# Kernel tuning notes

Hardware: AMD Instinct MI355X
Metric: run time of the kernel (lower is better)

The kernel has to match this reference:

```python
import jax, jax.numpy as jnp
import numpy as np

B, S, D = 1, 2048, 2048
H, G, HD = 32, 8, 64
EPS = 1e-6
ROPE_BASE = 10000.0


def rms_norm(x, g):
    # torch RMSNorm computed in fp32 then cast back (PytorchRMSNorm wrapper)
    xf = x.astype(jnp.float32)
    y = xf * jax.lax.rsqrt(jnp.mean(xf * xf, axis=-1, keepdims=True) + EPS) * g.astype(jnp.float32)
    return y.astype(x.dtype)


def rotate_half(x):
    x1, x2 = jnp.split(x, 2, axis=-1)
    return jnp.concatenate([-x2, x1], axis=-1)


def apply_rope(x, cos, sin):
    # x: (b, h, s, hd); cos/sin: (s, hd)
    return x * cos[None, None] + rotate_half(x) * sin[None, None]


def setup_inputs() -> dict:
    key = jax.random.key(0)
    ks = jax.random.split(key, 8)
    x = jax.random.normal(ks[0], (B, S, D), dtype=jnp.float32)
    wq = jax.random.normal(ks[1], (H * HD, D), dtype=jnp.float32) * (D ** -0.5)
    wk = jax.random.normal(ks[2], (G * HD, D), dtype=jnp.float32) * (D ** -0.5)
    wv = jax.random.normal(ks[3], (G * HD, D), dtype=jnp.float32) * (D ** -0.5)
    wo = jax.random.normal(ks[4], (D, H * HD), dtype=jnp.float32) * (D ** -0.5)
    qg = jnp.ones((HD,), dtype=jnp.float32)
    kg = jnp.ones((HD,), dtype=jnp.float32)
    # RoPE tables (HF-style: duplicated half-dim frequencies)
    inv_freq = 1.0 / (ROPE_BASE ** (jnp.arange(0, HD, 2, dtype=jnp.float32) / HD))
    ang = jnp.arange(S, dtype=jnp.float32)[:, None] * inv_freq[None, :]  # (S, HD/2)
    emb = jnp.concatenate([ang, ang], axis=-1)  # (S, HD)
    cos = jnp.cos(emb)
    sin = jnp.sin(emb)
    # causal mask: True = future (upper-right triangle)
    mask = jnp.triu(jnp.ones((S, S), dtype=bool), k=1)
    return {"x": x, "mask": mask, "cos": cos, "sin": sin,
            "wq": wq, "wk": wk, "wv": wv, "wo": wo, "qg": qg, "kg": kg}


def reference(x, mask, cos, sin, wq, wk, wv, wo, qg, kg):
    b, s, _ = x.shape
    rep = H // G
    q = (x @ wq.T).reshape(b, s, H, HD).transpose(0, 2, 1, 3)   # (b,H,s,hd)
    k = (x @ wk.T).reshape(b, s, G, HD).transpose(0, 2, 1, 3)   # (b,G,s,hd)
    v = (x @ wv.T).reshape(b, s, G, HD).transpose(0, 2, 1, 3)
    q = rms_norm(q, qg)
    k = rms_norm(k, kg)
    q = apply_rope(q, cos[:s], sin[:s])
    k = apply_rope(k, cos[:s], sin[:s])
    k = jnp.repeat(k, rep, axis=1)  # (b,H,s,hd) GQA expansion
    v = jnp.repeat(v, rep, axis=1)
    scores = jnp.einsum('bhqd,bhkd->bhqk', q, k) * (HD ** -0.5)
    neg = jnp.finfo(scores.dtype).min / 2
    scores = jnp.where(mask[None, None, :s, :s], neg, scores)
    w = jax.nn.softmax(scores, axis=-1)
    ctx = jnp.einsum('bhqk,bhkd->bhqd', w, v)
    ctx = ctx.transpose(0, 2, 1, 3).reshape(b, s, H * HD)
    return ctx @ wo.T
```

## Files before the change

kernel.cpp:

```cpp
#include <hip/hip_runtime.h>
#include <stdint.h>

#define SEQ    2048
#define DMODEL 2048
#define NHEAD  32
#define NKV    8
#define HDIM   64
#define NQKV   3072

typedef __bf16 bf16x8 __attribute__((ext_vector_type(8)));
typedef float  f32x4  __attribute__((ext_vector_type(4)));

#define SCALE2 0.180336880f
#define THR2   12.0f

__device__ __forceinline__ ushort bf(float f){
  __bf16 h = (__bf16)f;
  return __builtin_bit_cast(unsigned short, h);
}

__device__ __forceinline__ void gl_lds16(const void* g, void* l){
  __builtin_amdgcn_global_load_lds(
      (const __attribute__((address_space(1))) uint32_t*)g,
      (__attribute__((address_space(3))) uint32_t*)l, 16, 0, 0);
}

__global__ __launch_bounds__(256) void k_cvt_all(const float* __restrict__ x,
                                                 const float* __restrict__ wq,
                                                 const float* __restrict__ wk,
                                                 const float* __restrict__ wv,
                                                 const float* __restrict__ wo,
                                                 ushort* __restrict__ xb,
                                                 ushort* __restrict__ wcat,
                                                 ushort* __restrict__ wob){
  int i = blockIdx.x * 256 + threadIdx.x;
  const float* src; ushort* dst; int s4; int d4;
  if (i < 1048576)      { src = x;  dst = xb;   s4 = i;           d4 = s4; }
  else if (i < 2097152) { src = wq; dst = wcat; s4 = i - 1048576; d4 = s4; }
  else if (i < 2359296) { src = wk; dst = wcat; s4 = i - 2097152; d4 = s4 + 1048576; }
  else if (i < 2621440) { src = wv; dst = wcat; s4 = i - 2359296; d4 = s4 + 1310720; }
  else                  { src = wo; dst = wob;  s4 = i - 2621440; d4 = s4; }
  float4 v = reinterpret_cast<const float4*>(src)[s4];
  ushort4 o;
  o.x = bf(v.x); o.y = bf(v.y); o.z = bf(v.z); o.w = bf(v.w);
  reinterpret_cast<ushort4*>(dst)[d4] = o;
}

__global__ __launch_bounds__(256) void k_gemm_bt(const ushort* __restrict__ A,
                                                 const ushort* __restrict__ B,
                                                 float* __restrict__ C,
                                                 int M, int N, int K){
  __shared__ ushort As[2][128*64];
  __shared__ ushort Bs[2][128*64];
  const int tid = threadIdx.x, lane = tid & 63, wid = tid >> 6;
  const int bm = blockIdx.y * 128, bn = blockIdx.x * 128;
  const int wr = wid >> 1, wc = wid & 1;
  const int l15 = lane & 15, u = lane >> 4;

  const int srow = wid*32 + (lane >> 3);
  const int scol = ((lane & 7) ^ (lane >> 3)) * 8;
  const ushort* Abase = A + (size_t)(bm + srow) * K + scol;
  const ushort* Bbase = B + (size_t)(bn + srow) * K + scol;

  auto STAGE = [&](int buf, int k0){
#pragma unroll
    for (int c = 0; c < 4; c++){
      gl_lds16(Abase + k0 + (size_t)c*8*K, &As[buf][(wid*32 + c*8)*64]);
      gl_lds16(Bbase + k0 + (size_t)c*8*K, &Bs[buf][(wid*32 + c*8)*64]);
    }
  };

  f32x4 acc[4][4] = {};
  const int NT = K >> 6;

  STAGE(0, 0);
  __syncthreads();

  for (int t = 0; t < NT; t++){
    const int cur = t & 1;
    if (t + 1 < NT) STAGE(cur ^ 1, (t + 1) << 6);

#pragma unroll
    for (int kc = 0; kc < 2; kc++){
      bf16x8 af[4], bfr[4];
#pragma unroll
      for (int m = 0; m < 4; m++){
        int row = wr*64 + m*16 + l15;
        af[m] = *reinterpret_cast<const bf16x8*>(&As[cur][row*64 + (((kc*4+u) ^ (row&7))*8)]);
      }
#pragma unroll
      for (int n = 0; n < 4; n++){
        int row = wc*64 + n*16 + l15;
        bfr[n] = *reinterpret_cast<const bf16x8*>(&Bs[cur][row*64 + (((kc*4+u) ^ (row&7))*8)]);
      }
      __builtin_amdgcn_s_setprio(1);
#pragma unroll
      for (int m = 0; m < 4; m++)
#pragma unroll
        for (int n = 0; n < 4; n++)
          acc[m][n] = __builtin_amdgcn_mfma_f32_16x16x32_bf16(af[m], bfr[n], acc[m][n], 0, 0, 0);
      __builtin_amdgcn_s_setprio(0);
    }

    __syncthreads();
  }

#pragma unroll
  for (int m = 0; m < 4; m++)
#pragma unroll
    for (int n = 0; n < 4; n++)
#pragma unroll
      for (int j = 0; j < 4; j++){
        int row = bm + wr*64 + m*16 + u*4 + j;
        int col = bn + wc*64 + n*16 + l15;
        C[(size_t)row * N + col] = acc[m][n][j];
      }
}

__global__ __launch_bounds__(256) void k_normrope(const float* __restrict__ qkv,
                                                  const float* __restrict__ cosp,
                                                  const float* __restrict__ sinp,
                                                  const float* __restrict__ qg,
                                                  const float* __restrict__ kg,
                                                  ushort* __restrict__ qb,
                                                  ushort* __restrict__ kb){
  const int s = blockIdx.x;
  const int tid = threadIdx.x, lane = tid & 63, wid = tid >> 6;
  const float* row = qkv + (size_t)s * NQKV;
  const float cs = cosp[s*HDIM + lane];
  const float sn = sinp[s*HDIM + lane];

  for (int hidx = wid; hidx < 40; hidx += 4){
    const bool isq = hidx < 32;
    const int col = isq ? hidx*64 : 2048 + (hidx-32)*64;
    float x = row[col + lane];
    float ss = x * x;
#pragma unroll
    for (int m = 1; m < 64; m <<= 1) ss += __shfl_xor(ss, m);
    float r = rsqrtf(ss * (1.0f/64.0f) + 1e-6f);
    float y = x * r * (isq ? qg : kg)[lane];
    float p = __shfl_xor(y, 32);
    float out = y * cs + (lane < 32 ? -p : p) * sn;
    if (isq) qb[(size_t)s*2048 + hidx*64 + lane] = bf(out * SCALE2);
    else     kb[(size_t)s*512 + (hidx-32)*64 + lane] = bf(out);
  }
}

__global__ __launch_bounds__(256) void k_vtrans(const float* __restrict__ qkvf,
                                                ushort* __restrict__ vtb){
  __shared__ ushort tile[64][68];
  const int g = blockIdx.x >> 5, st = blockIdx.x & 31;
  const int tid = threadIdx.x;
#pragma unroll
  for (int i = 0; i < 4; i++){
    int idx = i*256 + tid;
    int r = idx >> 4, c4 = idx & 15;
    float4 v = *reinterpret_cast<const float4*>(
        qkvf + (size_t)(st*64 + r)*NQKV + 2560 + g*64 + c4*4);
    tile[c4*4+0][r] = bf(v.x);
    tile[c4*4+1][r] = bf(v.y);
    tile[c4*4+2][r] = bf(v.z);
    tile[c4*4+3][r] = bf(v.w);
  }
  __syncthreads();
#pragma unroll
  for (int i = 0; i < 4; i++){
    int idx = i*256 + tid;
    int d = idx >> 4, s4 = idx & 15;
    int pos4 = (s4 >> 3)*32 + (s4 & 3)*8 + ((s4 >> 2) & 1)*4;
    ushort4 o = *reinterpret_cast<const ushort4*>(&tile[d][s4*4]);
    *reinterpret_cast<ushort4*>(vtb + (size_t)(g*64 + d)*SEQ + st*64 + pos4) = o;
  }
}

__global__ __launch_bounds__(256) void k_attn(const ushort* __restrict__ qbuf,
                                              const ushort* __restrict__ kbuf,
                                              const ushort* __restrict__ vtb,
                                              ushort* __restrict__ ctx){
  __shared__ ushort Kd[2][64*64];
  __shared__ ushort Vd[2][64*64];

  const int bx = blockIdx.x;
  const int h  = bx & 31;
  const int qt = 31 - (bx >> 5);
  const int g = h >> 2;
  const int tid = threadIdx.x, lane = tid & 63, wid = tid >> 6;
  const int l15 = lane & 15, u = lane >> 4;
  const int q0 = qt*64 + wid*16;
  const int tmax = qt;

  bf16x8 qf[2];
#pragma unroll
  for (int kc = 0; kc < 2; kc++)
    qf[kc] = *reinterpret_cast<const bf16x8*>(
        qbuf + (size_t)(q0 + l15)*2048 + h*64 + kc*32 + u*8);

  f32x4 o[4] = {};
  float mrun = -1e30f;
  float lrun = 0.f;

  const int srow = wid*16 + (lane >> 3);
  const int scol = ((lane & 7) ^ (lane >> 3)) * 8;
  const ushort* ksrc0 = kbuf + (size_t)srow*512 + g*64 + scol;
  const ushort* vsrc0 = vtb  + (size_t)(g*64 + srow)*SEQ + scol;

  auto STAGE = [&](int buf, int t){
    const ushort* ks = ksrc0 + (size_t)t*64*512;
    gl_lds16(ks,         &Kd[buf][wid*1024]);
    gl_lds16(ks + 8*512, &Kd[buf][wid*1024 + 512]);
    const ushort* vs = vsrc0 + t*64;
    gl_lds16(vs,          &Vd[buf][wid*1024]);
    gl_lds16(vs + 8*SEQ,  &Vd[buf][wid*1024 + 512]);
  };

  STAGE(0, 0);
  __syncthreads();

  for (int t = 0; t <= tmax; t++){
    const int cur = t & 1;
    if (t < tmax) STAGE(cur ^ 1, t + 1);

    const ushort* Kb = &Kd[cur][0];
    const ushort* Vb = &Vd[cur][0];
    const bool full = (t*64 + 63) <= q0;

    f32x4 st[4];
#pragma unroll
    for (int kb = 0; kb < 4; kb++){
      const int key0 = t*64 + kb*16;
      const int keyl = kb*16 + l15;
      if (key0 <= q0 + 15){
        bf16x8 kf0 = *reinterpret_cast<const bf16x8*>(&Kb[keyl*64 + ((u     ^ (keyl&7))*8)]);
        bf16x8 kf1 = *reinterpret_cast<const bf16x8*>(&Kb[keyl*64 + (((4|u) ^ (keyl&7))*8)]);
        f32x4 a = {};
        a = __builtin_amdgcn_mfma_f32_16x16x32_bf16(kf0, qf[0], a, 0, 0, 0);
        a = __builtin_amdgcn_mfma_f32_16x16x32_bf16(kf1, qf[1], a, 0, 0, 0);
        st[kb] = a;
      } else {
        st[kb] = (f32x4){-1e30f, -1e30f, -1e30f, -1e30f};
      }
    }
    if (!full){
      const int keyb = t*64 + u*4;
      const int qr = q0 + l15;
#pragma unroll
      for (int kb = 0; kb < 4; kb++)
#pragma unroll
        for (int j = 0; j < 4; j++)
          st[kb][j] = (keyb + kb*16 + j > qr) ? -1e30f : st[kb][j];
    }

    {
      f32x4 mx = st[0];
#pragma unroll
      for (int kb = 1; kb < 4; kb++)
#pragma unroll
        for (int j = 0; j < 4; j++) mx[j] = fmaxf(mx[j], st[kb][j]);
      float tml = fmaxf(fmaxf(mx[0], mx[1]), fmaxf(mx[2], mx[3]));
      if (__any(tml > mrun + THR2)){
        float tm = fmaxf(tml, __shfl_xor(tml, 16));
        tm = fmaxf(tm, __shfl_xor(tm, 32));
        float mn = fmaxf(mrun, tm);
        float al = exp2f(mrun - mn);
        mrun = mn;
        lrun *= al;
#pragma unroll
        for (int d0 = 0; d0 < 4; d0++)
#pragma unroll
          for (int j = 0; j < 4; j++) o[d0][j] *= al;
      }

#pragma unroll
      for (int kb = 0; kb < 4; kb++)
#pragma unroll
        for (int j = 0; j < 4; j++){
          float p = exp2f(st[kb][j] - mrun);
          st[kb][j] = p;
          lrun += p;
        }
    }

    __builtin_amdgcn_s_setprio(1);
#pragma unroll
    for (int kc = 0; kc < 2; kc++){
      bf16x8 pb;
#pragma unroll
      for (int e = 0; e < 4; e++){
        pb[e]   = (__bf16)st[2*kc  ][e];
        pb[4+e] = (__bf16)st[2*kc+1][e];
      }
#pragma unroll
      for (int d0 = 0; d0 < 4; d0++){
        const int vrow = d0*16 + l15;
        bf16x8 vb8 = *reinterpret_cast<const bf16x8*>(
            &Vb[vrow*64 + (((kc*4+u) ^ (vrow&7))*8)]);
        o[d0] = __builtin_amdgcn_mfma_f32_16x16x32_bf16(vb8, pb, o[d0], 0, 0, 0);
      }
    }
    __builtin_amdgcn_s_setprio(0);

    __syncthreads();
  }

  {
    float lt = lrun + __shfl_xor(lrun, 16);
    lt += __shfl_xor(lt, 32);
    float inv = 1.0f / lt;
#pragma unroll
    for (int d0 = 0; d0 < 4; d0++){
      ushort4 w;
      w.x = bf(o[d0][0] * inv); w.y = bf(o[d0][1] * inv);
      w.z = bf(o[d0][2] * inv); w.w = bf(o[d0][3] * inv);
      *reinterpret_cast<ushort4*>(
          &ctx[(size_t)(q0 + l15)*2048 + h*64 + d0*16 + u*4]) = w;
    }
  }
}

extern "C" void kernel_launch(void* const* d_in, const int* in_sizes, int n_in,
                              void* d_out, int out_size, void* d_ws, size_t ws_size,
                              hipStream_t stream){
  const float* x    = (const float*)d_in[0];
  const float* cosp = (const float*)d_in[2];
  const float* sinp = (const float*)d_in[3];
  const float* wq   = (const float*)d_in[4];
  const float* wk   = (const float*)d_in[5];
  const float* wv   = (const float*)d_in[6];
  const float* wo   = (const float*)d_in[7];
  const float* qg   = (const float*)d_in[8];
  const float* kg   = (const float*)d_in[9];
  float* out = (float*)d_out;

  char* ws = (char*)d_ws;
  ushort* xb   = (ushort*)(ws);
  ushort* wcat = (ushort*)(ws + 8388608);
  ushort* wob  = (ushort*)(ws + 20971520);
  float*  qkvf = (float* )(ws + 29360128);
  ushort* qb   = (ushort*)(ws + 54525952);
  ushort* kb   = (ushort*)(ws + 62914560);
  ushort* vtb  = (ushort*)(ws + 65011712);
  ushort* ctxb = (ushort*)(ws + 67108864);

  k_cvt_all<<<14336, 256, 0, stream>>>(x, wq, wk, wv, wo, xb, wcat, wob);
  k_gemm_bt<<<dim3(24, 16), 256, 0, stream>>>(xb, wcat, qkvf, 2048, 3072, 2048);
  k_normrope<<<2048, 256, 0, stream>>>(qkvf, cosp, sinp, qg, kg, qb, kb);
  k_vtrans<<<256, 256, 0, stream>>>(qkvf, vtb);
  k_attn<<<1024, 256, 0, stream>>>(qb, kb, vtb, ctxb);
  k_gemm_bt<<<dim3(16, 16), 256, 0, stream>>>(ctxb, wob, out, 2048, 2048, 2048);
}
```

Measured before the change: 150.5 us.

## Store QKV projection in bf16, rebalance attention tile order, precompute LDS offsets

Adds a bf16-output variant of the QKV GEMM so the intermediate buffer is half the size, and updates normrope and vtrans to read bf16. This cuts global write and read traffic for the 2048x3072 intermediate, at the cost of rounding q/k to bf16 before RMSNorm. The attention kernel also gets a new block-to-query-tile mapping that interleaves long and short causal tiles for load balance. It also precomputes LDS fragment offsets and uses packed v_cvt_pk_bf16_f32 for the P conversion.

```diff
diff --git a/kernel.cpp b/kernel.cpp
--- a/kernel.cpp
+++ b/kernel.cpp
@@ -17,6 +17,9 @@
 __device__ __forceinline__ ushort bf(float f){
   __bf16 h = (__bf16)f;
   return __builtin_bit_cast(unsigned short, h);
+}
+__device__ __forceinline__ float b2f(ushort v){
+  union { uint32_t u; float f; } a; a.u = ((uint32_t)v) << 16; return a.f;
 }
 
 __device__ __forceinline__ void gl_lds16(const void* g, void* l){
@@ -117,7 +120,78 @@
       }
 }
 
-__global__ __launch_bounds__(256) void k_normrope(const float* __restrict__ qkv,
+__global__ __launch_bounds__(256) void k_gemm_btc(const ushort* __restrict__ A,
+                                                  const ushort* __restrict__ B,
+                                                  ushort* __restrict__ C,
+                                                  int M, int N, int K){
+  __shared__ ushort As[2][128*64];
+  __shared__ ushort Bs[2][128*64];
+  const int tid = threadIdx.x, lane = tid & 63, wid = tid >> 6;
+  const int bm = blockIdx.y * 128, bn = blockIdx.x * 128;
+  const int wr = wid >> 1, wc = wid & 1;
+  const int l15 = lane & 15, u = lane >> 4;
+
+  const int srow = wid*32 + (lane >> 3);
+  const int scol = ((lane & 7) ^ (lane >> 3)) * 8;
+  const ushort* Abase = A + (size_t)(bm + srow) * K + scol;
+  const ushort* Bbase = B + (size_t)(bn + srow) * K + scol;
+
+  auto STAGE = [&](int buf, int k0){
+#pragma unroll
+    for (int c = 0; c < 4; c++){
+      gl_lds16(Abase + k0 + (size_t)c*8*K, &As[buf][(wid*32 + c*8)*64]);
+      gl_lds16(Bbase + k0 + (size_t)c*8*K, &Bs[buf][(wid*32 + c*8)*64]);
+    }
+  };
+
+  f32x4 acc[4][4] = {};
+  const int NT = K >> 6;
+
+  STAGE(0, 0);
+  __syncthreads();
+
+  for (int t = 0; t < NT; t++){
+    const int cur = t & 1;
+    if (t + 1 < NT) STAGE(cur ^ 1, (t + 1) << 6);
+
+#pragma unroll
+    for (int kc = 0; kc < 2; kc++){
+      bf16x8 af[4], bfr[4];
+#pragma unroll
+      for (int m = 0; m < 4; m++){
+        int row = wr*64 + m*16 + l15;
+        af[m] = *reinterpret_cast<const bf16x8*>(&As[cur][row*64 + (((kc*4+u) ^ (row&7))*8)]);
+      }
+#pragma unroll
+      for (int n = 0; n < 4; n++){
+        int row = wc*64 + n*16 + l15;
+        bfr[n] = *reinterpret_cast<const bf16x8*>(&Bs[cur][row*64 + (((kc*4+u) ^ (row&7))*8)]);
+      }
+      __builtin_amdgcn_s_setprio(1);
+#pragma unroll
+      for (int m = 0; m < 4; m++)
+#pragma unroll
+        for (int n = 0; n < 4; n++)
+          acc[m][n] = __builtin_amdgcn_mfma_f32_16x16x32_bf16(af[m], bfr[n], acc[m][n], 0, 0, 0);
+      __builtin_amdgcn_s_setprio(0);
+    }
+
+    __syncthreads();
+  }
+
+#pragma unroll
+  for (int m = 0; m < 4; m++)
+#pragma unroll
+    for (int n = 0; n < 4; n++)
+#pragma unroll
+      for (int j = 0; j < 4; j++){
+        int row = bm + wr*64 + m*16 + u*4 + j;
+        int col = bn + wc*64 + n*16 + l15;
+        C[(size_t)row * N + col] = bf(acc[m][n][j]);
+      }
+}
+
+__global__ __launch_bounds__(256) void k_normrope(const ushort* __restrict__ qkvc,
                                                   const float* __restrict__ cosp,
                                                   const float* __restrict__ sinp,
                                                   const float* __restrict__ qg,
@@ -126,14 +200,14 @@
                                                   ushort* __restrict__ kb){
   const int s = blockIdx.x;
   const int tid = threadIdx.x, lane = tid & 63, wid = tid >> 6;
-  const float* row = qkv + (size_t)s * NQKV;
+  const ushort* row = qkvc + (size_t)s * NQKV;
   const float cs = cosp[s*HDIM + lane];
   const float sn = sinp[s*HDIM + lane];
 
   for (int hidx = wid; hidx < 40; hidx += 4){
     const bool isq = hidx < 32;
     const int col = isq ? hidx*64 : 2048 + (hidx-32)*64;
-    float x = row[col + lane];
+    float x = b2f(row[col + lane]);
     float ss = x * x;
 #pragma unroll
     for (int m = 1; m < 64; m <<= 1) ss += __shfl_xor(ss, m);
@@ -146,7 +220,7 @@
   }
 }
 
-__global__ __launch_bounds__(256) void k_vtrans(const float* __restrict__ qkvf,
+__global__ __launch_bounds__(256) void k_vtrans(const ushort* __restrict__ qkvc,
                                                 ushort* __restrict__ vtb){
   __shared__ ushort tile[64][68];
   const int g = blockIdx.x >> 5, st = blockIdx.x & 31;
@@ -155,12 +229,12 @@
   for (int i = 0; i < 4; i++){
     int idx = i*256 + tid;
     int r = idx >> 4, c4 = idx & 15;
-    float4 v = *reinterpret_cast<const float4*>(
-        qkvf + (size_t)(st*64 + r)*NQKV + 2560 + g*64 + c4*4);
-    tile[c4*4+0][r] = bf(v.x);
-    tile[c4*4+1][r] = bf(v.y);
-    tile[c4*4+2][r] = bf(v.z);
-    tile[c4*4+3][r] = bf(v.w);
+    ushort4 v = *reinterpret_cast<const ushort4*>(
+        qkvc + (size_t)(st*64 + r)*NQKV + 2560 + g*64 + c4*4);
+    tile[c4*4+0][r] = v.x;
+    tile[c4*4+1][r] = v.y;
+    tile[c4*4+2][r] = v.z;
+    tile[c4*4+3][r] = v.w;
   }
   __syncthreads();
 #pragma unroll
@@ -181,8 +255,10 @@
   __shared__ ushort Vd[2][64*64];
 
   const int bx = blockIdx.x;
-  const int h  = bx & 31;
-  const int qt = 31 - (bx >> 5);
+  const int c  = bx & 255, sl = bx >> 8;
+  const int cg = c >> 5,  h  = c & 31;
+  const int qt = (sl == 0) ? 31 - cg : (sl == 1) ? 16 + cg
+               : (sl == 2) ? 15 - cg : cg;
   const int g = h >> 2;
   const int tid = threadIdx.x, lane = tid & 63, wid = tid >> 6;
   const int l15 = lane & 15, u = lane >> 4;
@@ -198,6 +274,22 @@
   f32x4 o[4] = {};
   float mrun = -1e30f;
   float lrun = 0.f;
+
+  int koff[8], voff[8];
+#pragma unroll
+  for (int kb = 0; kb < 4; kb++)
+#pragma unroll
+    for (int kc = 0; kc < 2; kc++){
+      int keyl = kb*16 + l15;
+      koff[kb*2+kc] = (keyl*64 + (((kc*4+u) ^ (keyl&7))*8)) * 2;
+    }
+#pragma unroll
+  for (int kc = 0; kc < 2; kc++)
+#pragma unroll
+    for (int d0 = 0; d0 < 4; d0++){
+      int vrow = d0*16 + l15;
+      voff[kc*4+d0] = (vrow*64 + (((kc*4+u) ^ (vrow&7))*8)) * 2;
+    }
 
   const int srow = wid*16 + (lane >> 3);
   const int scol = ((lane & 7) ^ (lane >> 3)) * 8;
@@ -220,18 +312,17 @@
     const int cur = t & 1;
     if (t < tmax) STAGE(cur ^ 1, t + 1);
 
-    const ushort* Kb = &Kd[cur][0];
-    const ushort* Vb = &Vd[cur][0];
+    const char* KB = (const char*)Kd + cur*8192;
+    const char* VB = (const char*)Vd + cur*8192;
     const bool full = (t*64 + 63) <= q0;
 
     f32x4 st[4];
 #pragma unroll
     for (int kb = 0; kb < 4; kb++){
       const int key0 = t*64 + kb*16;
-      const int keyl = kb*16 + l15;
       if (key0 <= q0 + 15){
-        bf16x8 kf0 = *reinterpret_cast<const bf16x8*>(&Kb[keyl*64 + ((u     ^ (keyl&7))*8)]);
-        bf16x8 kf1 = *reinterpret_cast<const bf16x8*>(&Kb[keyl*64 + (((4|u) ^ (keyl&7))*8)]);
+        bf16x8 kf0 = *reinterpret_cast<const bf16x8*>(KB + koff[kb*2]);
+        bf16x8 kf1 = *reinterpret_cast<const bf16x8*>(KB + koff[kb*2+1]);
         f32x4 a = {};
         a = __builtin_amdgcn_mfma_f32_16x16x32_bf16(kf0, qf[0], a, 0, 0, 0);
         a = __builtin_amdgcn_mfma_f32_16x16x32_bf16(kf1, qf[1], a, 0, 0, 0);
@@ -269,7 +360,6 @@
 #pragma unroll
           for (int j = 0; j < 4; j++) o[d0][j] *= al;
       }
-
 #pragma unroll
       for (int kb = 0; kb < 4; kb++)
 #pragma unroll
@@ -283,18 +373,15 @@
     __builtin_amdgcn_s_setprio(1);
 #pragma unroll
     for (int kc = 0; kc < 2; kc++){
-      bf16x8 pb;
-#pragma unroll
-      for (int e = 0; e < 4; e++){
-        pb[e]   = (__bf16)st[2*kc  ][e];
-        pb[4+e] = (__bf16)st[2*kc+1][e];
-      }
+      union { uint32_t w[4]; bf16x8 v; } pb;
+      asm("v_cvt_pk_bf16_f32 %0, %1, %2" : "=v"(pb.w[0]) : "v"(st[2*kc  ][0]), "v"(st[2*kc  ][1]));
+      asm("v_cvt_pk_bf16_f32 %0, %1, %2" : "=v"(pb.w[1]) : "v"(st[2*kc  ][2]), "v"(st[2*kc  ][3]));
+      asm("v_cvt_pk_bf16_f32 %0, %1, %2" : "=v"(pb.w[2]) : "v"(st[2*kc+1][0]), "v"(st[2*kc+1][1]));
+      asm("v_cvt_pk_bf16_f32 %0, %1, %2" : "=v"(pb.w[3]) : "v"(st[2*kc+1][2]), "v"(st[2*kc+1][3]));
 #pragma unroll
       for (int d0 = 0; d0 < 4; d0++){
-        const int vrow = d0*16 + l15;
-        bf16x8 vb8 = *reinterpret_cast<const bf16x8*>(
-            &Vb[vrow*64 + (((kc*4+u) ^ (vrow&7))*8)]);
-        o[d0] = __builtin_amdgcn_mfma_f32_16x16x32_bf16(vb8, pb, o[d0], 0, 0, 0);
+        bf16x8 vb8 = *reinterpret_cast<const bf16x8*>(VB + voff[kc*4+d0]);
+        o[d0] = __builtin_amdgcn_mfma_f32_16x16x32_bf16(vb8, pb.v, o[d0], 0, 0, 0);
       }
     }
     __builtin_amdgcn_s_setprio(0);
@@ -335,16 +422,16 @@
   ushort* xb   = (ushort*)(ws);
   ushort* wcat = (ushort*)(ws + 8388608);
   ushort* wob  = (ushort*)(ws + 20971520);
-  float*  qkvf = (float* )(ws + 29360128);
-  ushort* qb   = (ushort*)(ws + 54525952);
-  ushort* kb   = (ushort*)(ws + 62914560);
-  ushort* vtb  = (ushort*)(ws + 65011712);
-  ushort* ctxb = (ushort*)(ws + 67108864);
+  ushort* qkvc = (ushort*)(ws + 29360128);
+  ushort* qb   = (ushort*)(ws + 41943040);
+  ushort* kb   = (ushort*)(ws + 50331648);
+  ushort* vtb  = (ushort*)(ws + 52428800);
+  ushort* ctxb = (ushort*)(ws + 54525952);
 
   k_cvt_all<<<14336, 256, 0, stream>>>(x, wq, wk, wv, wo, xb, wcat, wob);
-  k_gemm_bt<<<dim3(24, 16), 256, 0, stream>>>(xb, wcat, qkvf, 2048, 3072, 2048);
-  k_normrope<<<2048, 256, 0, stream>>>(qkvf, cosp, sinp, qg, kg, qb, kb);
-  k_vtrans<<<256, 256, 0, stream>>>(qkvf, vtb);
+  k_gemm_btc<<<dim3(24, 16), 256, 0, stream>>>(xb, wcat, qkvc, 2048, 3072, 2048);
+  k_normrope<<<2048, 256, 0, stream>>>(qkvc, cosp, sinp, qg, kg, qb, kb);
+  k_vtrans<<<256, 256, 0, stream>>>(qkvc, vtb);
   k_attn<<<1024, 256, 0, stream>>>(qb, kb, vtb, ctxb);
   k_gemm_bt<<<dim3(16, 16), 256, 0, stream>>>(ctxb, wob, out, 2048, 2048, 2048);
 }
```

After: 150.5 us. No clear change (-0.0%).
